# Performance work log

Measured on AMD Instinct MI355X. Metric: run time of the kernel, lower is better.

## Reference

```python
import jax, jax.numpy as jnp
import numpy as np

B, S, E = 4, 2048, 1024
H, D = 16, 64
SCALE = D ** -0.5


def setup_inputs() -> dict:
    key = jax.random.key(0)
    ks = jax.random.split(key, 6)
    x = jax.random.normal(ks[0], (B, S, E), dtype=jnp.float32)
    # per-head projection weights stacked along head axis: [H, E, D]
    Wq = jax.random.normal(ks[1], (H, E, D), dtype=jnp.float32) * 0.02
    Wk = jax.random.normal(ks[2], (H, E, D), dtype=jnp.float32) * 0.02
    Wv = jax.random.normal(ks[3], (H, E, D), dtype=jnp.float32) * 0.02
    # output projection: concat(H*D) -> E, with bias (nn.Linear default)
    Wo = jax.random.normal(ks[4], (H * D, E), dtype=jnp.float32) * 0.02
    bo = jax.random.normal(ks[5], (E,), dtype=jnp.float32) * 0.02
    return {"x": x, "Wq": Wq, "Wk": Wk, "Wv": Wv, "Wo": Wo, "bo": bo}


def reference(x, Wq, Wk, Wv, Wo, bo):
    # batched QKV projections for all heads at once
    q = jnp.einsum('bse,hed->bhsd', x, Wq)
    k = jnp.einsum('bse,hed->bhsd', x, Wk)
    v = jnp.einsum('bse,hed->bhsd', x, Wv)
    # full (non-causal) attention, scores [b,h,s,s]
    scores = jnp.einsum('bhsd,bhtd->bhst', q, k) * SCALE
    attn = jax.nn.softmax(scores, axis=-1)
    o = jnp.einsum('bhst,bhtd->bhsd', attn, v)
    # concat heads in head order along feature dim -> [b,s,H*D]
    o = o.transpose(0, 2, 1, 3).reshape(x.shape[0], x.shape[1], -1)
    return o @ Wo + bo
```

## Files before the change

### kernel.cpp

```cpp
#include <hip/hip_runtime.h>
#include <hip/hip_fp16.h>
#include <stdint.h>

#define BB 4
#define SS 2048
#define EE 1024
#define HH 16
#define DD 64

typedef _Float16 half8 __attribute__((ext_vector_type(8)));
typedef __fp16 fp16x2 __attribute__((ext_vector_type(2)));
typedef float f32x4 __attribute__((ext_vector_type(4)));
typedef float f32x16 __attribute__((ext_vector_type(16)));
typedef uint32_t u32;
typedef uint32_t u32x2 __attribute__((ext_vector_type(2)));

#define MFMA32(a, b, c) __builtin_amdgcn_mfma_f32_16x16x32_f16((a), (b), (c), 0, 0, 0)
#define MFMA3216(a, b, c) __builtin_amdgcn_mfma_f32_32x32x16_f16((a), (b), (c), 0, 0, 0)

#define GLD_LDS16(g, l)                                                        \
  __builtin_amdgcn_global_load_lds(                                            \
      (const __attribute__((address_space(1))) u32*)(const void*)(g),          \
      (__attribute__((address_space(3))) u32*)(void*)(l), 16, 0, 0)

static __device__ __forceinline__ u32 pkh(float a, float b) {
  union { fp16x2 h; u32 u; } z;
  z.h = __builtin_amdgcn_cvt_pkrtz(a, b);
  return z.u;
}

static __device__ __forceinline__ void plswap(u32& a, u32& b) {
  asm("v_permlane32_swap_b32 %0, %1" : "+v"(a), "+v"(b));
}

__global__ __launch_bounds__(256) void conv_x_k(const float* __restrict__ x,
                                                _Float16* __restrict__ xh) {
  size_t i = ((size_t)blockIdx.x * 256 + threadIdx.x) * 8;
  f32x4 a = *(const f32x4*)(x + i);
  f32x4 b = *(const f32x4*)(x + i + 4);
  half8 o;
  o[0] = (_Float16)a[0]; o[1] = (_Float16)a[1];
  o[2] = (_Float16)a[2]; o[3] = (_Float16)a[3];
  o[4] = (_Float16)b[0]; o[5] = (_Float16)b[1];
  o[6] = (_Float16)b[2]; o[7] = (_Float16)b[3];
  *(half8*)(xh + i) = o;
}

__global__ __launch_bounds__(256) void conv_w_k(const float* __restrict__ Wq,
                                                const float* __restrict__ Wk,
                                                const float* __restrict__ Wv,
                                                _Float16* __restrict__ Wt) {
  __shared__ float T[64][65];
  int bid = blockIdx.x;
  int sel = bid >> 8, rem = bid & 255;
  int h = rem >> 4, e0 = (rem & 15) * 64;
  const float* W = (sel == 0 ? Wq : sel == 1 ? Wk : Wv) + (size_t)h * EE * DD;
  float scale = (sel == 0) ? 0.18033688011112042f : 1.0f;
  int tid = threadIdx.x;
  {
    int e = tid >> 2, d0 = (tid & 3) * 16;
#pragma unroll
    for (int i = 0; i < 4; ++i) {
      f32x4 v = *(const f32x4*)(W + (size_t)(e0 + e) * DD + d0 + i * 4);
      T[e][d0 + i * 4 + 0] = v[0];
      T[e][d0 + i * 4 + 1] = v[1];
      T[e][d0 + i * 4 + 2] = v[2];
      T[e][d0 + i * 4 + 3] = v[3];
    }
  }
  __syncthreads();
  {
    int d = tid >> 2, c0 = (tid & 3) * 16;
    half8 o0, o1;
#pragma unroll
    for (int i = 0; i < 8; ++i) o0[i] = (_Float16)(T[c0 + i][d] * scale);
#pragma unroll
    for (int i = 0; i < 8; ++i) o1[i] = (_Float16)(T[c0 + 8 + i][d] * scale);
    _Float16* dst = Wt + ((size_t)sel * 1024 + h * 64 + d) * EE + e0 + c0;
    *(half8*)dst = o0;
    *(half8*)(dst + 8) = o1;
  }
}

__global__ __launch_bounds__(256) void conv_wo_k(const float* __restrict__ Wo,
                                                 _Float16* __restrict__ Wot) {
  __shared__ float T[64][65];
  int bid = blockIdx.x;
  int k0 = (bid >> 4) * 64, n0 = (bid & 15) * 64;
  int tid = threadIdx.x;
  {
    int k = tid >> 2, c0 = (tid & 3) * 16;
#pragma unroll
    for (int i = 0; i < 4; ++i) {
      f32x4 v = *(const f32x4*)(Wo + (size_t)(k0 + k) * EE + n0 + c0 + i * 4);
      T[k][c0 + i * 4 + 0] = v[0];
      T[k][c0 + i * 4 + 1] = v[1];
      T[k][c0 + i * 4 + 2] = v[2];
      T[k][c0 + i * 4 + 3] = v[3];
    }
  }
  __syncthreads();
  {
    int n = tid >> 2, c0 = (tid & 3) * 16;
    half8 o0, o1;
#pragma unroll
    for (int i = 0; i < 8; ++i) o0[i] = (_Float16)T[c0 + i][n];
#pragma unroll
    for (int i = 0; i < 8; ++i) o1[i] = (_Float16)T[c0 + 8 + i][n];
    _Float16* dst = Wot + (size_t)(n0 + n) * EE + k0 + c0;
    *(half8*)dst = o0;
    *(half8*)(dst + 8) = o1;
  }
}

__global__ __launch_bounds__(256) void vtrans_k(const _Float16* __restrict__ v,
                                                _Float16* __restrict__ vT) {
  __shared__ _Float16 T[64][72];
  int bid = blockIdx.x;
  int bh = bid >> 5, st = bid & 31;
  const _Float16* vp = v + (size_t)bh * SS * DD + (size_t)st * 64 * DD;
  _Float16* op = vT + (size_t)bh * DD * SS + (size_t)st * 64;
  int tid = threadIdx.x;
  {
    int r = tid >> 2, c0 = (tid & 3) * 16;
    half8 a = *(const half8*)(vp + (size_t)r * DD + c0);
    half8 b = *(const half8*)(vp + (size_t)r * DD + c0 + 8);
#pragma unroll
    for (int j = 0; j < 8; ++j) T[c0 + j][r] = a[j];
#pragma unroll
    for (int j = 0; j < 8; ++j) T[c0 + 8 + j][r] = b[j];
  }
  __syncthreads();
  {
    int d = tid >> 2, sc = (tid & 3) * 16;
    half8 o0 = *(const half8*)&T[d][sc];
    half8 o1 = *(const half8*)&T[d][sc + 8];
    *(half8*)(op + (size_t)d * SS + sc) = o0;
    *(half8*)(op + (size_t)d * SS + sc + 8) = o1;
  }
}

__global__ __launch_bounds__(256, 3) void qkv_proj_k(
    const _Float16* __restrict__ xh, const _Float16* __restrict__ Wt,
    _Float16* __restrict__ qkv) {
  __shared__ __align__(16) _Float16 As[128 * 32];
  __shared__ __align__(16) _Float16 Bs[128 * 32];
  int bid0 = blockIdx.x;
  int bid = (bid0 & 7) * 192 + (bid0 >> 3);
  int nblk = bid % 24, mblk = bid / 24;
  int row0 = mblk * 128, n0 = nblk * 128;
  int tid = threadIdx.x, lane = tid & 63, w = tid >> 6;
  int wm = w >> 1, wn = w & 1;
  int l15 = lane & 15, lhi = lane >> 4;

  f32x4 acc[4][4];
#pragma unroll
  for (int i = 0; i < 4; ++i)
#pragma unroll
    for (int j = 0; j < 4; ++j) acc[i][j] = (f32x4){0.f, 0.f, 0.f, 0.f};

  const char* Ab = (const char*)xh + (size_t)row0 * 2048;
  const char* Bb = (const char*)Wt + (size_t)n0 * 2048;
  int ob0 = w * 1024 + lane * 16;

  for (int k0 = 0; k0 < EE; k0 += 32) {
    __syncthreads();
    GLD_LDS16(Ab + (size_t)(ob0 >> 6) * 2048 + k0 * 2 + (ob0 & 63),
              (char*)As + w * 1024);
    GLD_LDS16(Ab + (size_t)((ob0 + 4096) >> 6) * 2048 + k0 * 2 + (ob0 & 63),
              (char*)As + 4096 + w * 1024);
    GLD_LDS16(Bb + (size_t)(ob0 >> 6) * 2048 + k0 * 2 + (ob0 & 63),
              (char*)Bs + w * 1024);
    GLD_LDS16(Bb + (size_t)((ob0 + 4096) >> 6) * 2048 + k0 * 2 + (ob0 & 63),
              (char*)Bs + 4096 + w * 1024);
    __syncthreads();
    half8 a[4], b[4];
#pragma unroll
    for (int mf = 0; mf < 4; ++mf)
      a[mf] = *(const half8*)(As + (wm * 64 + mf * 16 + l15) * 32 + 8 * lhi);
#pragma unroll
    for (int nf = 0; nf < 4; ++nf)
      b[nf] = *(const half8*)(Bs + (wn * 64 + nf * 16 + l15) * 32 + 8 * lhi);
#pragma unroll
    for (int mf = 0; mf < 4; ++mf)
#pragma unroll
      for (int nf = 0; nf < 4; ++nf)
        acc[mf][nf] = MFMA32(a[mf], b[nf], acc[mf][nf]);
  }

  const size_t KOFF = (size_t)BB * HH * SS * DD;
#pragma unroll
  for (int mf = 0; mf < 4; ++mf)
#pragma unroll
    for (int nf = 0; nf < 4; ++nf)
#pragma unroll
      for (int r = 0; r < 4; ++r) {
        int row = row0 + wm * 64 + mf * 16 + 4 * lhi + r;
        int n = n0 + wn * 64 + nf * 16 + l15;
        int sel = n >> 10, hh = (n >> 6) & 15, d = n & 63;
        int b_ = row >> 11, s = row & 2047;
        qkv[(size_t)sel * KOFF + (((size_t)b_ * HH + hh) * SS + s) * DD + d] =
            (_Float16)acc[mf][nf][r];
      }
}

__global__ __launch_bounds__(128, 4) void attn_k(
    const _Float16* __restrict__ qkv, const _Float16* __restrict__ vT,
    _Float16* __restrict__ ob) {
  __shared__ __align__(16) _Float16 Ks[2][64 * 64];
  __shared__ __align__(16) _Float16 Vs[2][64 * 64];

  const int bid0 = blockIdx.x;
  const int bid = (bid0 & 7) * 128 + (bid0 >> 3);
  const int bh = bid >> 4, qb = bid & 15;
  const int b_ = bh >> 4, h = bh & 15;
  const size_t KOFF = (size_t)BB * HH * SS * DD;
  const _Float16* qp = qkv + (size_t)bh * SS * DD;
  const char* kp = (const char*)(qkv + KOFF + (size_t)bh * SS * DD);
  const char* vtp = (const char*)(vT + (size_t)bh * DD * SS);

  const int tid = threadIdx.x, lane = tid & 63, w = tid >> 6;
  const int l31 = lane & 31, u = lane >> 5;
  const int q0 = qb * 128 + w * 64;

  half8 qf[4][2];
#pragma unroll
  for (int ekf = 0; ekf < 4; ++ekf)
#pragma unroll
    for (int nq = 0; nq < 2; ++nq)
      qf[ekf][nq] = *(const half8*)(qp +
          (size_t)(q0 + nq * 32 + l31) * DD + ekf * 16 + u * 8);

  f32x16 oa00 = {}, oa10 = {}, oa01 = {}, oa11 = {};
  float rs0 = 0.f, rs1 = 0.f;

  const int trow = tid >> 3;
  const int scol = ((tid & 7) * 16) ^ (16 * (trow & 7));
  const int lds0 = tid * 16;
  const int xsw = 16 * (l31 & 7);
  const int NT = SS / 64;

#pragma unroll
  for (int j = 0; j < 4; ++j) {
    GLD_LDS16(kp + (trow + 16 * j) * 128 + scol, (char*)Ks[0] + j * 2048 + lds0);
    GLD_LDS16(vtp + (size_t)(trow + 16 * j) * 4096 + scol,
              (char*)Vs[0] + j * 2048 + lds0);
  }
  __syncthreads();

  for (int it = 0; it < NT; ++it) {
    const int cur = it & 1;
    if (it + 1 < NT) {
      const char* kn = kp + (size_t)(it + 1) * 8192;
      const char* vn = vtp + (size_t)(it + 1) * 128;
#pragma unroll
      for (int j = 0; j < 4; ++j) {
        GLD_LDS16(kn + (trow + 16 * j) * 128 + scol,
                  (char*)Ks[cur ^ 1] + j * 2048 + lds0);
        GLD_LDS16(vn + (size_t)(trow + 16 * j) * 4096 + scol,
                  (char*)Vs[cur ^ 1] + j * 2048 + lds0);
      }
    }
    const char* kb = (const char*)Ks[cur];
    const char* vb = (const char*)Vs[cur];

#pragma unroll
    for (int nt = 0; nt < 2; ++nt) {
      const char* krow = kb + (size_t)(32 * nt + l31) * 128;
      half8 kA0 = *(const half8*)(krow + ((16 * u) ^ xsw));
      half8 kA1 = *(const half8*)(krow + ((32 + 16 * u) ^ xsw));
      half8 kA2 = *(const half8*)(krow + ((64 + 16 * u) ^ xsw));
      half8 kA3 = *(const half8*)(krow + ((96 + 16 * u) ^ xsw));
      f32x16 s0 = {}, s1 = {};
      __builtin_amdgcn_s_setprio(1);
      s0 = MFMA3216(kA0, qf[0][0], s0);
      s1 = MFMA3216(kA0, qf[0][1], s1);
      s0 = MFMA3216(kA1, qf[1][0], s0);
      s1 = MFMA3216(kA1, qf[1][1], s1);
      s0 = MFMA3216(kA2, qf[2][0], s0);
      s1 = MFMA3216(kA2, qf[2][1], s1);
      s0 = MFMA3216(kA3, qf[3][0], s0);
      s1 = MFMA3216(kA3, qf[3][1], s1);
      __builtin_amdgcn_s_setprio(0);

      u32 w0[8], w1[8];
#pragma unroll
      for (int m = 0; m < 8; ++m) {
        float a0 = __builtin_amdgcn_exp2f(s0[2 * m]);
        float a1 = __builtin_amdgcn_exp2f(s0[2 * m + 1]);
        rs0 += a0 + a1;
        w0[m] = pkh(a0, a1);
        float c0 = __builtin_amdgcn_exp2f(s1[2 * m]);
        float c1 = __builtin_amdgcn_exp2f(s1[2 * m + 1]);
        rs1 += c0 + c1;
        w1[m] = pkh(c0, c1);
      }

#pragma unroll
      for (int kfl = 0; kfl < 2; ++kfl) {
        u32 p00 = w0[4 * kfl + 0], p02 = w0[4 * kfl + 2];
        u32 p01 = w0[4 * kfl + 1], p03 = w0[4 * kfl + 3];
        plswap(p00, p02);
        plswap(p01, p03);
        u32 p10 = w1[4 * kfl + 0], p12 = w1[4 * kfl + 2];
        u32 p11 = w1[4 * kfl + 1], p13 = w1[4 * kfl + 3];
        plswap(p10, p12);
        plswap(p11, p13);
        union { u32 q[4]; half8 h; } pb0, pb1;
        pb0.q[0] = p00; pb0.q[1] = p01; pb0.q[2] = p02; pb0.q[3] = p03;
        pb1.q[0] = p10; pb1.q[1] = p11; pb1.q[2] = p12; pb1.q[3] = p13;
        const int kf = 2 * nt + kfl;
        const char* vcol = vb + ((32 * kf + 16 * u) ^ xsw);
        half8 vA0 = *(const half8*)(vcol + (size_t)l31 * 128);
        half8 vA1 = *(const half8*)(vcol + (size_t)(32 + l31) * 128);
        __builtin_amdgcn_s_setprio(1);
        oa00 = MFMA3216(vA0, pb0.h, oa00);
        oa10 = MFMA3216(vA1, pb0.h, oa10);
        oa01 = MFMA3216(vA0, pb1.h, oa01);
        oa11 = MFMA3216(vA1, pb1.h, oa11);
        __builtin_amdgcn_s_setprio(0);
      }
    }
    __syncthreads();
  }

  float inv0 = 1.0f / (rs0 + __shfl_xor(rs0, 32, 64));
  float inv1 = 1.0f / (rs1 + __shfl_xor(rs1, 32, 64));

#define STORE_OA(OA, MD, NQ, INV)                                              \
  {                                                                            \
    _Float16* dst = ob + (size_t)(b_ * SS + q0 + 32 * (NQ) + l31) * 1024 +     \
                    h * 64 + 32 * (MD) + 4 * u;                                \
    _Pragma("unroll")                                                          \
    for (int rr = 0; rr < 4; ++rr) {                                           \
      u32x2 pr;                                                                \
      pr.x = pkh(OA[4 * rr + 0] * (INV), OA[4 * rr + 1] * (INV));              \
      pr.y = pkh(OA[4 * rr + 2] * (INV), OA[4 * rr + 3] * (INV));              \
      *(u32x2*)(dst + 8 * rr) = pr;                                            \
    }                                                                          \
  }
  STORE_OA(oa00, 0, 0, inv0)
  STORE_OA(oa10, 1, 0, inv0)
  STORE_OA(oa01, 0, 1, inv1)
  STORE_OA(oa11, 1, 1, inv1)
#undef STORE_OA
}

__global__ __launch_bounds__(256, 3) void oproj_k(
    const _Float16* __restrict__ ob, const _Float16* __restrict__ Wot,
    const float* __restrict__ bo, float* __restrict__ out) {
  __shared__ __align__(16) _Float16 As[128 * 32];
  __shared__ __align__(16) _Float16 Bs[128 * 32];
  int bid0 = blockIdx.x;
  int bid = (bid0 & 7) * 64 + (bid0 >> 3);
  int nblk = bid & 7, mblk = bid >> 3;
  int row0 = mblk * 128, n0 = nblk * 128;
  int tid = threadIdx.x, lane = tid & 63, w = tid >> 6;
  int wm = w >> 1, wn = w & 1;
  int l15 = lane & 15, lhi = lane >> 4;

  f32x4 acc[4][4];
#pragma unroll
  for (int i = 0; i < 4; ++i)
#pragma unroll
    for (int j = 0; j < 4; ++j) acc[i][j] = (f32x4){0.f, 0.f, 0.f, 0.f};

  const char* Ab = (const char*)ob + (size_t)row0 * 2048;
  const char* Bb = (const char*)Wot + (size_t)n0 * 2048;
  int ob0 = w * 1024 + lane * 16;

  for (int k0 = 0; k0 < EE; k0 += 32) {
    __syncthreads();
    GLD_LDS16(Ab + (size_t)(ob0 >> 6) * 2048 + k0 * 2 + (ob0 & 63),
              (char*)As + w * 1024);
    GLD_LDS16(Ab + (size_t)((ob0 + 4096) >> 6) * 2048 + k0 * 2 + (ob0 & 63),
              (char*)As + 4096 + w * 1024);
    GLD_LDS16(Bb + (size_t)(ob0 >> 6) * 2048 + k0 * 2 + (ob0 & 63),
              (char*)Bs + w * 1024);
    GLD_LDS16(Bb + (size_t)((ob0 + 4096) >> 6) * 2048 + k0 * 2 + (ob0 & 63),
              (char*)Bs + 4096 + w * 1024);
    __syncthreads();
    half8 a[4], b[4];
#pragma unroll
    for (int mf = 0; mf < 4; ++mf)
      a[mf] = *(const half8*)(As + (wm * 64 + mf * 16 + l15) * 32 + 8 * lhi);
#pragma unroll
    for (int nf = 0; nf < 4; ++nf)
      b[nf] = *(const half8*)(Bs + (wn * 64 + nf * 16 + l15) * 32 + 8 * lhi);
#pragma unroll
    for (int mf = 0; mf < 4; ++mf)
#pragma unroll
      for (int nf = 0; nf < 4; ++nf)
        acc[mf][nf] = MFMA32(a[mf], b[nf], acc[mf][nf]);
  }

#pragma unroll
  for (int mf = 0; mf < 4; ++mf)
#pragma unroll
    for (int nf = 0; nf < 4; ++nf) {
      int n = n0 + wn * 64 + nf * 16 + l15;
      float bias = bo[n];
#pragma unroll
      for (int r = 0; r < 4; ++r) {
        int row = row0 + wm * 64 + mf * 16 + 4 * lhi + r;
        out[(size_t)row * EE + n] = acc[mf][nf][r] + bias;
      }
    }
}

extern "C" void kernel_launch(void* const* d_in, const int* in_sizes, int n_in,
                              void* d_out, int out_size, void* d_ws, size_t ws_size,
                              hipStream_t stream) {
  const float* x  = (const float*)d_in[0];
  const float* Wq = (const float*)d_in[1];
  const float* Wk = (const float*)d_in[2];
  const float* Wv = (const float*)d_in[3];
  const float* Wo = (const float*)d_in[4];
  const float* bo = (const float*)d_in[5];
  float* out = (float*)d_out;

  const size_t KOFF = (size_t)BB * HH * SS * DD;
  _Float16* qkv = (_Float16*)d_ws;
  _Float16* obuf = qkv + 3 * KOFF;
  _Float16* xh = (_Float16*)d_out;
  _Float16* Wt = xh + (size_t)BB * SS * EE;
  _Float16* vTbuf = xh;
  _Float16* Wot = qkv;

  conv_x_k<<<dim3(4096), dim3(256), 0, stream>>>(x, xh);
  conv_w_k<<<dim3(768), dim3(256), 0, stream>>>(Wq, Wk, Wv, Wt);
  qkv_proj_k<<<dim3(64 * 24), dim3(256), 0, stream>>>(xh, Wt, qkv);
  vtrans_k<<<dim3(64 * 32), dim3(256), 0, stream>>>(qkv + 2 * KOFF, vTbuf);
  attn_k<<<dim3(64 * 16), dim3(128), 0, stream>>>(qkv, vTbuf, obuf);
  conv_wo_k<<<dim3(256), dim3(256), 0, stream>>>(Wo, Wot);
  oproj_k<<<dim3(64 * 8), dim3(256), 0, stream>>>(obuf, Wot, bo, out);
}
```

Measured before the change: 210.2 us.

## Widen attention blocks to 8 waves sharing each K/V tile

The attention kernel now runs 512-thread blocks of 8 waves covering 512 query rows per (batch, head), where before it used 128-thread blocks of 2 waves. Each K/V tile load is therefore shared by four times as many waves, and each thread issues one async global-to-LDS copy per tile instead of four. The grid drops to 256 blocks with one block per CU allowed, which cuts global K/V traffic but leaves fewer resident waves to hide latency and puts more waves on each barrier. Row-sum accumulation also switches to a packed two-wide float vector, aiming for packed-math adds.

```diff
diff --git a/kernel.cpp b/kernel.cpp
--- a/kernel.cpp
+++ b/kernel.cpp
@@ -10,6 +10,7 @@
 
 typedef _Float16 half8 __attribute__((ext_vector_type(8)));
 typedef __fp16 fp16x2 __attribute__((ext_vector_type(2)));
+typedef float f32x2 __attribute__((ext_vector_type(2)));
 typedef float f32x4 __attribute__((ext_vector_type(4)));
 typedef float f32x16 __attribute__((ext_vector_type(16)));
 typedef uint32_t u32;
@@ -204,15 +205,15 @@
       }
 }
 
-__global__ __launch_bounds__(128, 4) void attn_k(
+__global__ __launch_bounds__(512, 1) void attn_k(
     const _Float16* __restrict__ qkv, const _Float16* __restrict__ vT,
     _Float16* __restrict__ ob) {
   __shared__ __align__(16) _Float16 Ks[2][64 * 64];
   __shared__ __align__(16) _Float16 Vs[2][64 * 64];
 
   const int bid0 = blockIdx.x;
-  const int bid = (bid0 & 7) * 128 + (bid0 >> 3);
-  const int bh = bid >> 4, qb = bid & 15;
+  const int bid = (bid0 & 7) * 32 + (bid0 >> 3);
+  const int bh = bid >> 2, qb = bid & 3;
   const int b_ = bh >> 4, h = bh & 15;
   const size_t KOFF = (size_t)BB * HH * SS * DD;
   const _Float16* qp = qkv + (size_t)bh * SS * DD;
@@ -221,7 +222,7 @@
 
   const int tid = threadIdx.x, lane = tid & 63, w = tid >> 6;
   const int l31 = lane & 31, u = lane >> 5;
-  const int q0 = qb * 128 + w * 64;
+  const int q0 = qb * 512 + w * 64;
 
   half8 qf[4][2];
 #pragma unroll
@@ -232,7 +233,7 @@
           (size_t)(q0 + nq * 32 + l31) * DD + ekf * 16 + u * 8);
 
   f32x16 oa00 = {}, oa10 = {}, oa01 = {}, oa11 = {};
-  float rs0 = 0.f, rs1 = 0.f;
+  f32x2 rs2_0 = {0.f, 0.f}, rs2_1 = {0.f, 0.f};
 
   const int trow = tid >> 3;
   const int scol = ((tid & 7) * 16) ^ (16 * (trow & 7));
@@ -240,26 +241,17 @@
   const int xsw = 16 * (l31 & 7);
   const int NT = SS / 64;
 
-#pragma unroll
-  for (int j = 0; j < 4; ++j) {
-    GLD_LDS16(kp + (trow + 16 * j) * 128 + scol, (char*)Ks[0] + j * 2048 + lds0);
-    GLD_LDS16(vtp + (size_t)(trow + 16 * j) * 4096 + scol,
-              (char*)Vs[0] + j * 2048 + lds0);
-  }
+  GLD_LDS16(kp + trow * 128 + scol, (char*)Ks[0] + lds0);
+  GLD_LDS16(vtp + (size_t)trow * 4096 + scol, (char*)Vs[0] + lds0);
   __syncthreads();
 
   for (int it = 0; it < NT; ++it) {
     const int cur = it & 1;
     if (it + 1 < NT) {
-      const char* kn = kp + (size_t)(it + 1) * 8192;
-      const char* vn = vtp + (size_t)(it + 1) * 128;
-#pragma unroll
-      for (int j = 0; j < 4; ++j) {
-        GLD_LDS16(kn + (trow + 16 * j) * 128 + scol,
-                  (char*)Ks[cur ^ 1] + j * 2048 + lds0);
-        GLD_LDS16(vn + (size_t)(trow + 16 * j) * 4096 + scol,
-                  (char*)Vs[cur ^ 1] + j * 2048 + lds0);
-      }
+      GLD_LDS16(kp + (size_t)(it + 1) * 8192 + trow * 128 + scol,
+                (char*)Ks[cur ^ 1] + lds0);
+      GLD_LDS16(vtp + (size_t)(it + 1) * 128 + (size_t)trow * 4096 + scol,
+                (char*)Vs[cur ^ 1] + lds0);
     }
     const char* kb = (const char*)Ks[cur];
     const char* vb = (const char*)Vs[cur];
@@ -288,12 +280,12 @@
       for (int m = 0; m < 8; ++m) {
         float a0 = __builtin_amdgcn_exp2f(s0[2 * m]);
         float a1 = __builtin_amdgcn_exp2f(s0[2 * m + 1]);
-        rs0 += a0 + a1;
         w0[m] = pkh(a0, a1);
+        rs2_0 += (f32x2){a0, a1};
         float c0 = __builtin_amdgcn_exp2f(s1[2 * m]);
         float c1 = __builtin_amdgcn_exp2f(s1[2 * m + 1]);
-        rs1 += c0 + c1;
         w1[m] = pkh(c0, c1);
+        rs2_1 += (f32x2){c0, c1};
       }
 
 #pragma unroll
@@ -324,6 +316,8 @@
     __syncthreads();
   }
 
+  float rs0 = rs2_0.x + rs2_0.y;
+  float rs1 = rs2_1.x + rs2_1.y;
   float inv0 = 1.0f / (rs0 + __shfl_xor(rs0, 32, 64));
   float inv1 = 1.0f / (rs1 + __shfl_xor(rs1, 32, 64));
 
@@ -431,7 +425,7 @@
   conv_w_k<<<dim3(768), dim3(256), 0, stream>>>(Wq, Wk, Wv, Wt);
   qkv_proj_k<<<dim3(64 * 24), dim3(256), 0, stream>>>(xh, Wt, qkv);
   vtrans_k<<<dim3(64 * 32), dim3(256), 0, stream>>>(qkv + 2 * KOFF, vTbuf);
-  attn_k<<<dim3(64 * 16), dim3(128), 0, stream>>>(qkv, vTbuf, obuf);
+  attn_k<<<dim3(256), dim3(512), 0, stream>>>(qkv, vTbuf, obuf);
   conv_wo_k<<<dim3(256), dim3(256), 0, stream>>>(Wo, Wot);
   oproj_k<<<dim3(64 * 8), dim3(256), 0, stream>>>(obuf, Wot, bo, out);
 }
```

Result: faster. 196.9 us (-6.3%).
